# Performance work log

Hardware: AMD Instinct MI355X
Metric: run time of the kernel (lower is better)

## Reference

```python
import jax, jax.numpy as jnp
import numpy as np

D_MODEL = 64      # init_kwargs d_model
MAX_RANGE = 1.0   # init_kwargs max_range
N_POINTS = 1_000_000


def _positional_encoding(n):
    # encoding[i, 2j]   = sin(i / 10000**(2j/d_model))
    # encoding[i, 2j+1] = cos(i / 10000**(2j/d_model))
    i = jnp.arange(n, dtype=jnp.float32)[:, None]                 # [N, 1]
    j = jnp.arange(D_MODEL // 2, dtype=jnp.float32)[None, :]      # [1, D/2]
    pos_val = i / jnp.power(jnp.float32(10000.0), 2.0 * j / D_MODEL)  # [N, D/2]
    enc = jnp.stack([jnp.sin(pos_val), jnp.cos(pos_val)], axis=-1)    # [N, D/2, 2]
    enc = enc.reshape(n, 2 * (D_MODEL // 2))
    if 2 * (D_MODEL // 2) < D_MODEL:  # odd d_model: last column stays zero
        enc = jnp.pad(enc, ((0, 0), (0, D_MODEL - 2 * (D_MODEL // 2))))
    return MAX_RANGE * enc


def setup_inputs() -> dict:
    key = jax.random.key(0)
    point_cloud = jax.random.normal(key, (N_POINTS, 6), dtype=jnp.float32)
    return {"point_cloud": point_cloud}


def reference(point_cloud):
    n = point_cloud.shape[0]
    coords = point_cloud[:, :3]
    colours = point_cloud[:, 3:]
    enc = _positional_encoding(n)
    return jnp.concatenate([coords, enc, colours], axis=1)  # [N, 6 + d_model]
```

## Files before the change

### kernel.cpp

```cpp
#include <hip/hip_runtime.h>
#include <math.h>


#define ROWS_PER_BLOCK 64
#define OUTC 70
#define FLOATS_PER_BLOCK (ROWS_PER_BLOCK * OUTC)
#define VEC4_PER_BLOCK   (FLOATS_PER_BLOCK / 4)
#define IN_FLOATS_PER_BLOCK (ROWS_PER_BLOCK * 6)
#define IN_VEC4_PER_BLOCK   (IN_FLOATS_PER_BLOCK/4)

__global__ __launch_bounds__(256, 8) void pe_kernel(const float* __restrict__ pc,
                                                    float* __restrict__ out,
                                                    int n_rows) {
    __shared__ float s_tile[FLOATS_PER_BLOCK];

    const int tid = threadIdx.x;
    const int b = blockIdx.x;
    const int rowBase = b * ROWS_PER_BLOCK;

    const int j = tid & 31;
    double w = 0.15915494309189533577;
    if (j & 1)  w *= 0.74989420933245585;
    if (j & 2)  w *= 0.5623413251903491;
    if (j & 4)  w *= 0.31622776601683794;
    if (j & 8)  w *= 0.1;
    if (j & 16) w *= 0.01;

    const long long in_total = (long long)n_rows * 6;
    float4 vin;
    bool fast_in = false;
    long long f0 = 0;
    if (tid < IN_VEC4_PER_BLOCK) {
        const long long inBase = (long long)b * IN_FLOATS_PER_BLOCK;
        f0 = inBase + tid * 4;
        if (f0 + 3 < in_total) {
            vin = reinterpret_cast<const float4*>(pc)[inBase / 4 + tid];
            fast_in = true;
        }
    }

    int r = tid >> 5;
#pragma unroll 4
    for (int k = 0; k < 8; ++k) {
        const double t = (double)(rowBase + r) * w;
        const double frac = t - rint(t);
        const float fr = (float)frac;
        const int pos = r * OUTC + 3 + 2 * j;
        s_tile[pos]     = __builtin_amdgcn_sinf(fr);
        s_tile[pos + 1] = __builtin_amdgcn_cosf(fr);
        r += 8;
    }

    if (tid < IN_VEC4_PER_BLOCK) {
        if (fast_in) {
            const float* ve = &vin.x;
#pragma unroll
            for (int m = 0; m < 4; ++m) {
                const int fl = tid * 4 + m;
                const int row = fl / 6;
                const int c = fl - row * 6;
                const int col = (c < 3) ? c : (c + 64);
                s_tile[row * OUTC + col] = ve[m];
            }
        } else {
            for (int m = 0; m < 4; ++m) {
                const long long f = f0 + m;
                if (f < in_total) {
                    const float val = pc[f];
                    const int fl = tid * 4 + m;
                    const int row = fl / 6;
                    const int c = fl - row * 6;
                    const int col = (c < 3) ? c : (c + 64);
                    s_tile[row * OUTC + col] = val;
                }
            }
        }
    }
    __syncthreads();

    const long long outBase = (long long)b * FLOATS_PER_BLOCK;
    const long long total = (long long)n_rows * OUTC;
    float4* __restrict__ out4 = reinterpret_cast<float4*>(out);
    if (outBase + FLOATS_PER_BLOCK <= total) {
        for (int i = tid; i < VEC4_PER_BLOCK; i += 256) {
            float4 v;
            v.x = s_tile[i * 4 + 0];
            v.y = s_tile[i * 4 + 1];
            v.z = s_tile[i * 4 + 2];
            v.w = s_tile[i * 4 + 3];
            out4[outBase / 4 + i] = v;
        }
    } else {
        for (int i = tid; i < VEC4_PER_BLOCK; i += 256) {
            const long long g = outBase + (long long)i * 4;
            if (g + 4 <= total) {
                float4 v;
                v.x = s_tile[i * 4 + 0];
                v.y = s_tile[i * 4 + 1];
                v.z = s_tile[i * 4 + 2];
                v.w = s_tile[i * 4 + 3];
                out4[outBase / 4 + i] = v;
            } else {
                for (int m = 0; m < 4; ++m)
                    if (g + m < total) out[g + m] = s_tile[i * 4 + m];
            }
        }
    }
}

extern "C" void kernel_launch(void* const* d_in, const int* in_sizes, int n_in,
                              void* d_out, int out_size, void* d_ws, size_t ws_size,
                              hipStream_t stream) {
    const float* pc = (const float*)d_in[0];
    float* out = (float*)d_out;
    const int n_rows = in_sizes[0] / 6;
    const int grid = (n_rows + ROWS_PER_BLOCK - 1) / ROWS_PER_BLOCK;
    pe_kernel<<<dim3(grid), dim3(256), 0, stream>>>(pc, out, n_rows);
}
```

Measured before the change: 297.2 us.

## Use persistent blocks with double-buffered LDS tiles to overlap compute and stores

Replaces the one-block-per-64-row launch with a capped grid of persistent blocks, each looping over contiguous 32-row tiles. Two shared-memory buffers let the next tile's input prefetch and sin/cos computation proceed while the current tile is written out. This is meant to cut launch and tail overhead and hide compute behind the store stream of a write-bound kernel. In exchange it adds a loop with a barrier per tile, lowers the number of waves in flight, and uses smaller tiles per store burst.

```diff
diff --git a/kernel.cpp b/kernel.cpp
--- a/kernel.cpp
+++ b/kernel.cpp
@@ -2,21 +2,118 @@
 #include <math.h>
 
 
-#define ROWS_PER_BLOCK 64
+#define TILE_ROWS 32
 #define OUTC 70
-#define FLOATS_PER_BLOCK (ROWS_PER_BLOCK * OUTC)
-#define VEC4_PER_BLOCK   (FLOATS_PER_BLOCK / 4)
-#define IN_FLOATS_PER_BLOCK (ROWS_PER_BLOCK * 6)
-#define IN_VEC4_PER_BLOCK   (IN_FLOATS_PER_BLOCK/4)
+#define TILE_FLOATS (TILE_ROWS * OUTC)
+#define TILE_V4     (TILE_FLOATS / 4)
+#define TILE_IN     (TILE_ROWS * 6)
+#define TILE_IN_V4  (TILE_IN / 4)
+#define BLOCK 256
+#define MAX_GRID 2048
+
+__device__ __forceinline__ void prefetch_in(const float* __restrict__ pc, int t,
+                                            long long in_total, int tid,
+                                            float4& vin, bool& fast, long long& f0) {
+    fast = false; f0 = 0;
+    if (tid < TILE_IN_V4) {
+        const long long inBase = (long long)t * TILE_IN;
+        f0 = inBase + tid * 4;
+        if (f0 + 3 < in_total) {
+            vin = reinterpret_cast<const float4*>(pc)[inBase / 4 + tid];
+            fast = true;
+        }
+    }
+}
+
+__device__ __forceinline__ void compute_enc(float* __restrict__ buf, int t,
+                                            int tid, int j, double w) {
+    const int rowBase = t * TILE_ROWS;
+    int r = tid >> 5;
+#pragma unroll
+    for (int k = 0; k < 4; ++k) {
+        const double tt = (double)(rowBase + r) * w;
+        const double frac = tt - rint(tt);
+        const float fr = (float)frac;
+        const int pos = r * OUTC + 3 + 2 * j;
+        buf[pos]     = __builtin_amdgcn_sinf(fr);
+        buf[pos + 1] = __builtin_amdgcn_cosf(fr);
+        r += 8;
+    }
+}
+
+__device__ __forceinline__ void scatter_in(float* __restrict__ buf,
+                                           const float* __restrict__ pc,
+                                           long long in_total, int tid,
+                                           const float4& vin, bool fast, long long f0) {
+    if (tid < TILE_IN_V4) {
+        if (fast) {
+            const float* ve = &vin.x;
+#pragma unroll
+            for (int m = 0; m < 4; ++m) {
+                const int fl = tid * 4 + m;
+                const int row = fl / 6;
+                const int c = fl - row * 6;
+                const int col = (c < 3) ? c : (c + 64);
+                buf[row * OUTC + col] = ve[m];
+            }
+        } else {
+            for (int m = 0; m < 4; ++m) {
+                const long long f = f0 + m;
+                if (f < in_total) {
+                    const float val = pc[f];
+                    const int fl = tid * 4 + m;
+                    const int row = fl / 6;
+                    const int c = fl - row * 6;
+                    const int col = (c < 3) ? c : (c + 64);
+                    buf[row * OUTC + col] = val;
+                }
+            }
+        }
+    }
+}
+
+__device__ __forceinline__ void store_tile(const float* __restrict__ buf,
+                                           float* __restrict__ out, int t,
+                                           long long total, int tid) {
+    const long long outBase = (long long)t * TILE_FLOATS;
+    float4* __restrict__ out4 = reinterpret_cast<float4*>(out);
+    if (outBase + TILE_FLOATS <= total) {
+        for (int i = tid; i < TILE_V4; i += BLOCK) {
+            float4 v;
+            v.x = buf[i * 4 + 0];
+            v.y = buf[i * 4 + 1];
+            v.z = buf[i * 4 + 2];
+            v.w = buf[i * 4 + 3];
+            out4[outBase / 4 + i] = v;
+        }
+    } else {
+        for (int i = tid; i < TILE_V4; i += BLOCK) {
+            const long long g = outBase + (long long)i * 4;
+            if (g + 4 <= total) {
+                float4 v;
+                v.x = buf[i * 4 + 0];
+                v.y = buf[i * 4 + 1];
+                v.z = buf[i * 4 + 2];
+                v.w = buf[i * 4 + 3];
+                out4[outBase / 4 + i] = v;
+            } else {
+                for (int m = 0; m < 4; ++m)
+                    if (g + m < total) out[g + m] = buf[i * 4 + m];
+            }
+        }
+    }
+}
 
 __global__ __launch_bounds__(256, 8) void pe_kernel(const float* __restrict__ pc,
                                                     float* __restrict__ out,
-                                                    int n_rows) {
-    __shared__ float s_tile[FLOATS_PER_BLOCK];
+                                                    int n_rows, int tiles_per_block) {
+    __shared__ float s_tile[2][TILE_FLOATS];
 
     const int tid = threadIdx.x;
-    const int b = blockIdx.x;
-    const int rowBase = b * ROWS_PER_BLOCK;
+    const int T = (n_rows + TILE_ROWS - 1) / TILE_ROWS;
+    const int t0 = blockIdx.x * tiles_per_block;
+    const int t1 = (t0 + tiles_per_block < T) ? (t0 + tiles_per_block) : T;
+    if (t0 >= t1) return;
 
     const int j = tid & 31;
     double w = 0.15915494309189533577;
@@ -27,84 +124,28 @@
     if (j & 16) w *= 0.01;
 
     const long long in_total = (long long)n_rows * 6;
-    float4 vin;
-    bool fast_in = false;
-    long long f0 = 0;
-    if (tid < IN_VEC4_PER_BLOCK) {
-        const long long inBase = (long long)b * IN_FLOATS_PER_BLOCK;
-        f0 = inBase + tid * 4;
-        if (f0 + 3 < in_total) {
-            vin = reinterpret_cast<const float4*>(pc)[inBase / 4 + tid];
-            fast_in = true;
-        }
-    }
+    const long long total    = (long long)n_rows * OUTC;
 
-    int r = tid >> 5;
-#pragma unroll 4
-    for (int k = 0; k < 8; ++k) {
-        const double t = (double)(rowBase + r) * w;
-        const double frac = t - rint(t);
-        const float fr = (float)frac;
-        const int pos = r * OUTC + 3 + 2 * j;
-        s_tile[pos]     = __builtin_amdgcn_sinf(fr);
-        s_tile[pos + 1] = __builtin_amdgcn_cosf(fr);
-        r += 8;
-    }
-
-    if (tid < IN_VEC4_PER_BLOCK) {
-        if (fast_in) {
-            const float* ve = &vin.x;
-#pragma unroll
-            for (int m = 0; m < 4; ++m) {
-                const int fl = tid * 4 + m;
-                const int row = fl / 6;
-                const int c = fl - row * 6;
-                const int col = (c < 3) ? c : (c + 64);
-                s_tile[row * OUTC + col] = ve[m];
-            }
-        } else {
-            for (int m = 0; m < 4; ++m) {
-                const long long f = f0 + m;
-                if (f < in_total) {
-                    const float val = pc[f];
-                    const int fl = tid * 4 + m;
-                    const int row = fl / 6;
-                    const int c = fl - row * 6;
-                    const int col = (c < 3) ? c : (c + 64);
-                    s_tile[row * OUTC + col] = val;
-                }
-            }
-        }
+    {
+        float4 vin; bool fast; long long f0;
+        prefetch_in(pc, t0, in_total, tid, vin, fast, f0);
+        compute_enc(s_tile[0], t0, tid, j, w);
+        scatter_in(s_tile[0], pc, in_total, tid, vin, fast, f0);
     }
     __syncthreads();
 
-    const long long outBase = (long long)b * FLOATS_PER_BLOCK;
-    const long long total = (long long)n_rows * OUTC;
-    float4* __restrict__ out4 = reinterpret_cast<float4*>(out);
-    if (outBase + FLOATS_PER_BLOCK <= total) {
-        for (int i = tid; i < VEC4_PER_BLOCK; i += 256) {
-            float4 v;
-            v.x = s_tile[i * 4 + 0];
-            v.y = s_tile[i * 4 + 1];
-            v.z = s_tile[i * 4 + 2];
-            v.w = s_tile[i * 4 + 3];
-            out4[outBase / 4 + i] = v;
+    int cur = 0;
+    for (int t = t0; t < t1; ++t) {
+        const bool has_next = (t + 1 < t1);
+        float4 vin; bool fast = false; long long f0 = 0;
+        if (has_next) prefetch_in(pc, t + 1, in_total, tid, vin, fast, f0);
+        store_tile(s_tile[cur], out, t, total, tid);
+        if (has_next) {
+            compute_enc(s_tile[cur ^ 1], t + 1, tid, j, w);
+            scatter_in(s_tile[cur ^ 1], pc, in_total, tid, vin, fast, f0);
         }
-    } else {
-        for (int i = tid; i < VEC4_PER_BLOCK; i += 256) {
-            const long long g = outBase + (long long)i * 4;
-            if (g + 4 <= total) {
-                float4 v;
-                v.x = s_tile[i * 4 + 0];
-                v.y = s_tile[i * 4 + 1];
-                v.z = s_tile[i * 4 + 2];
-                v.w = s_tile[i * 4 + 3];
-                out4[outBase / 4 + i] = v;
-            } else {
-                for (int m = 0; m < 4; ++m)
-                    if (g + m < total) out[g + m] = s_tile[i * 4 + m];
-            }
-        }
+        __syncthreads();
+        cur ^= 1;
     }
 }
 
@@ -114,6 +155,9 @@
     const float* pc = (const float*)d_in[0];
     float* out = (float*)d_out;
     const int n_rows = in_sizes[0] / 6;
-    const int grid = (n_rows + ROWS_PER_BLOCK - 1) / ROWS_PER_BLOCK;
-    pe_kernel<<<dim3(grid), dim3(256), 0, stream>>>(pc, out, n_rows);
+    const int T = (n_rows + TILE_ROWS - 1) / TILE_ROWS;
+    int grid = (T < MAX_GRID) ? T : MAX_GRID;
+    const int tpb = (T + grid - 1) / grid;
+    grid = (T + tpb - 1) / tpb;
+    pe_kernel<<<dim3(grid), dim3(BLOCK), 0, stream>>>(pc, out, n_rows, tpb);
 }
```

New measurement: 304.2 us. 2.4% more time.
